# Kernel optimization log

Hardware: AMD Instinct MI355X
Metric: run time of the kernel (lower is better)

## Reference

```python
import jax, jax.numpy as jnp
import numpy as np

B, T, D, H = 8, 1024, 768, 12
HD = D // H          # 64 head dim
WINDOW = 768         # sliding-window width hardcoded in the block
EPS = 1e-5

def _layer_norm(x, w, b):
    mu = jnp.mean(x, axis=-1, keepdims=True)
    var = jnp.mean(jnp.square(x - mu), axis=-1, keepdims=True)
    return (x - mu) * jax.lax.rsqrt(var + EPS) * w + b

def setup_inputs() -> dict:
    key = jax.random.key(0)
    ks = jax.random.split(key, 16)
    s = 0.02
    return {
        "x": jax.random.normal(ks[0], (B, T, D), jnp.float32),
        "attn_mask": jnp.ones((B, T), jnp.int32),
        "ln1_w": jnp.ones((D,), jnp.float32),
        "ln1_b": jnp.zeros((D,), jnp.float32),
        "w_attn": jax.random.normal(ks[1], (D, 3 * D), jnp.float32) * s,
        "b_attn": jnp.zeros((3 * D,), jnp.float32),
        "w_proj": jax.random.normal(ks[2], (D, D), jnp.float32) * s,
        "b_proj": jnp.zeros((D,), jnp.float32),
        "ln2_w": jnp.ones((D,), jnp.float32),
        "ln2_b": jnp.zeros((D,), jnp.float32),
        "w_fc": jax.random.normal(ks[3], (D, 4 * D), jnp.float32) * s,
        "b_fc": jnp.zeros((4 * D,), jnp.float32),
        "w_fc_proj": jax.random.normal(ks[4], (4 * D, D), jnp.float32) * s,
        "b_fc_proj": jnp.zeros((D,), jnp.float32),
    }

def reference(x, attn_mask, ln1_w, ln1_b, w_attn, b_attn, w_proj, b_proj,
              ln2_w, ln2_b, w_fc, b_fc, w_fc_proj, b_fc_proj):
    dtype = x.dtype
    # --- attention sub-block ---
    x1 = _layer_norm(x, ln1_w, ln1_b)
    qkv = x1 @ w_attn + b_attn                       # [B,T,3D]
    q, k, v = jnp.split(qkv, 3, axis=-1)
    q = q.reshape(B, T, H, HD).transpose(0, 2, 1, 3)  # [B,H,T,HD]
    k = k.reshape(B, T, H, HD).transpose(0, 2, 1, 3)
    v = v.reshape(B, T, H, HD).transpose(0, 2, 1, 3)
    # causal + sliding-window + padding mask (additive bias, as in source)
    i = jnp.arange(T)[:, None]
    j = jnp.arange(T)[None, :]
    keep = (j <= i) & (j >= i - WINDOW + 1)           # [T,T]
    keep = keep[None, None] & (attn_mask.astype(bool))[:, None, None, :]  # [B,1,T,T]
    mask_bias = jnp.where(keep, jnp.zeros((), dtype), jnp.full((), jnp.finfo(dtype).min, dtype))
    scale = 1.0 / np.sqrt(HD)
    scores = jnp.einsum('bhqd,bhkd->bhqk', q, k) * scale + mask_bias
    probs = jax.nn.softmax(scores, axis=-1)
    attn = jnp.einsum('bhqk,bhkd->bhqd', probs, v)    # [B,H,T,HD]
    attn = attn.transpose(0, 2, 1, 3).reshape(B, T, D)
    a = attn @ w_proj + b_proj
    x = x + a
    # --- MLP sub-block ---
    x3 = _layer_norm(x, ln2_w, ln2_b)
    h = jax.nn.gelu(x3 @ w_fc + b_fc, approximate=False)
    m = h @ w_fc_proj + b_fc_proj
    return x + m
```

## Files before the change

kernel.cpp:

```cpp
#include <hip/hip_runtime.h>
#include <hip/hip_bf16.h>
#include <math.h>

#define NB 8
#define NT 1024
#define ND 768
#define NH 12
#define HD 64
#define WINDOW 768
#define LN_EPS 1e-5f
#define NEGF -3.4028234663852886e38f
#define SCL2 0.18033688011112042f

static const int BT = NB * NT;

typedef __bf16 bf16x8 __attribute__((ext_vector_type(8)));
typedef float  f32x4  __attribute__((ext_vector_type(4)));
typedef unsigned short ushort_t;

__device__ __forceinline__ unsigned short f2bf(float f) {
    __hip_bfloat16 h = __float2bfloat16(f);
    return __builtin_bit_cast(unsigned short, h);
}

__device__ __forceinline__ void load_lds16(const void* g, void* l) {
    __builtin_amdgcn_global_load_lds((const __attribute__((address_space(1))) unsigned int*)g,
                                     (__attribute__((address_space(3))) unsigned int*)l,
                                     16, 0, 0);
}

template <int IMM>
__device__ __forceinline__ bf16x8 ds_read16o(unsigned base) {
    bf16x8 r;
    asm volatile("ds_read_b128 %0, %1 offset:%2" : "=v"(r) : "v"(base), "n"(IMM));
    return r;
}

__global__ __launch_bounds__(256) void transpose_all(const float* __restrict__ w0, ushort_t* __restrict__ t0v,
                                                     const float* __restrict__ w1, ushort_t* __restrict__ t1v,
                                                     const float* __restrict__ w2, ushort_t* __restrict__ t2v,
                                                     const float* __restrict__ w3, ushort_t* __restrict__ t3v) {
    int bid = blockIdx.x;
    const float* w; ushort_t* wt; int K, N;
    if (bid < 1728)                    { w = w0; wt = t0v; K = 768;  N = 2304; }
    else if ((bid -= 1728) < 576)      { w = w1; wt = t1v; K = 768;  N = 768;  }
    else if ((bid -= 576) < 2304)      { w = w2; wt = t2v; K = 768;  N = 3072; }
    else       { bid -= 2304;            w = w3; wt = t3v; K = 3072; N = 768;  }
    const int nxt = N / 32;
    const int n0 = (bid % nxt) * 32, k0 = (bid / nxt) * 32;
    __shared__ float t[32][33];
    const int tx = threadIdx.x & 31, ty = threadIdx.x >> 5;
    for (int r = ty; r < 32; r += 8)
        t[r][tx] = w[(size_t)(k0 + r) * N + n0 + tx];
    __syncthreads();
    for (int r = ty; r < 32; r += 8)
        wt[(size_t)(n0 + r) * K + k0 + tx] = f2bf(t[tx][r]);
}

__global__ __launch_bounds__(256) void transpose_v(const ushort_t* __restrict__ qkvb,
                                                   ushort_t* __restrict__ vT) {
    const int t0 = blockIdx.x * 64;
    const int h = blockIdx.y, b = blockIdx.z;
    __shared__ ushort_t sm[64 * 72];
    const int tid = threadIdx.x;
    #pragma unroll
    for (int p = 0; p < 2; p++) {
        int idx = p * 256 + tid;
        int r = idx >> 3, c = idx & 7;
        *(bf16x8*)&sm[r * 72 + c * 8] =
            *(const bf16x8*)(qkvb + (size_t)(b * NT + t0 + r) * (3 * ND) + 2 * ND + h * HD + c * 8);
    }
    __syncthreads();
    #pragma unroll
    for (int p = 0; p < 2; p++) {
        int idx = p * 256 + tid;
        int d = idx >> 3, c2 = idx & 7;
        ushort_t tmp[8];
        #pragma unroll
        for (int j = 0; j < 8; j++) {
            int kp = c2 * 8 + j;
            int key = ((kp & 1) << 4) | ((kp >> 1) & 15) | (kp & 32);
            tmp[j] = sm[key * 72 + d];
        }
        *(bf16x8*)(vT + ((size_t)((b * NH + h) * HD + d)) * NT + t0 + c2 * 8) = *(bf16x8*)tmp;
    }
}

__global__ __launch_bounds__(256) void ln_kernel(const float* __restrict__ x,
                                                 const float* __restrict__ w,
                                                 const float* __restrict__ b,
                                                 ushort_t* __restrict__ out) {
    const int row  = blockIdx.x * 4 + (threadIdx.x >> 6);
    const int lane = threadIdx.x & 63;
    const float* xr = x + (size_t)row * ND;

    float4 v[3];
    #pragma unroll
    for (int s = 0; s < 3; s++) v[s] = *(const float4*)(xr + s * 256 + lane * 4);

    float sum = 0.f;
    #pragma unroll
    for (int s = 0; s < 3; s++) sum += v[s].x + v[s].y + v[s].z + v[s].w;
    #pragma unroll
    for (int off = 1; off < 64; off <<= 1) sum += __shfl_xor(sum, off, 64);
    const float mu = sum * (1.0f / ND);

    float var = 0.f;
    #pragma unroll
    for (int s = 0; s < 3; s++) {
        float a0 = v[s].x - mu, a1 = v[s].y - mu, a2 = v[s].z - mu, a3 = v[s].w - mu;
        var += a0 * a0 + a1 * a1 + a2 * a2 + a3 * a3;
    }
    #pragma unroll
    for (int off = 1; off < 64; off <<= 1) var += __shfl_xor(var, off, 64);
    const float rstd = rsqrtf(var * (1.0f / ND) + LN_EPS);

    #pragma unroll
    for (int s = 0; s < 3; s++) {
        const int col = s * 256 + lane * 4;
        float4 w4 = *(const float4*)(w + col);
        float4 b4 = *(const float4*)(b + col);
        ushort4 r;
        r.x = f2bf((v[s].x - mu) * rstd * w4.x + b4.x);
        r.y = f2bf((v[s].y - mu) * rstd * w4.y + b4.y);
        r.z = f2bf((v[s].z - mu) * rstd * w4.z + b4.z);
        r.w = f2bf((v[s].w - mu) * rstd * w4.w + b4.w);
        *(ushort4*)(out + (size_t)row * ND + col) = r;
    }
}

template <int EPI>
__global__ __launch_bounds__(256) void gemm_bt(const ushort_t* __restrict__ A,
                                               const ushort_t* __restrict__ Bt,
                                               const float* __restrict__ bias,
                                               const float* __restrict__ resid,
                                               void* __restrict__ Cout,
                                               int M, int N, int K) {
    __shared__ __align__(16) ushort_t smem[2][2][128 * 32];

    const int tid  = threadIdx.x;
    const int nwg   = gridDim.x * gridDim.y;
    const int flatb = blockIdx.y * gridDim.x + blockIdx.x;
    const int q8    = nwg >> 3;
    const int swz   = (flatb & 7) * q8 + (flatb >> 3);
    const int bm   = (swz / gridDim.x) * 128;
    const int bn   = (swz % gridDim.x) * 128;
    const int lane = tid & 63;
    const int wave = tid >> 6;
    const int wm   = (wave & 1) * 64;
    const int wn   = (wave >> 1) * 64;
    const int fcol = lane & 15;
    const int quad = lane >> 4;

    f32x4 acc[4][4] = {};

    const int srow = tid >> 2, scg = (tid & 3) * 8;

    auto issue = [&](int k0, int buf) {
        #pragma unroll
        for (int p = 0; p < 2; p++) {
            const int row = srow + p * 64;
            const int flat = (p * 256 + tid) * 8;
            load_lds16(A  + (size_t)(bm + row) * K + k0 + scg, &smem[buf][0][flat]);
            load_lds16(Bt + (size_t)(bn + row) * K + k0 + scg, &smem[buf][1][flat]);
        }
    };

    issue(0, 0);
    const int KT = K >> 5;
    for (int kt = 0; kt < KT; kt++) {
        const int cur = kt & 1;
        __syncthreads();
        if (kt + 1 < KT) issue((kt + 1) << 5, cur ^ 1);

        bf16x8 a[4], b[4];
        #pragma unroll
        for (int i = 0; i < 4; i++)
            a[i] = *(const bf16x8*)&smem[cur][0][(wm + i * 16 + fcol) * 32 + quad * 8];
        #pragma unroll
        for (int j = 0; j < 4; j++)
            b[j] = *(const bf16x8*)&smem[cur][1][(wn + j * 16 + fcol) * 32 + quad * 8];
        #pragma unroll
        for (int i = 0; i < 4; i++)
            #pragma unroll
            for (int j = 0; j < 4; j++)
                acc[i][j] = __builtin_amdgcn_mfma_f32_16x16x32_bf16(a[i], b[j], acc[i][j], 0, 0, 0);
    }

    if (EPI == 1) {
        #pragma unroll
        for (int j = 0; j < 4; j++) {
            const int gcol = bn + wn + j * 16 + fcol;
            const float bs = bias[gcol];
            #pragma unroll
            for (int i = 0; i < 4; i++) {
                #pragma unroll
                for (int r = 0; r < 4; r++) {
                    const int grow = bm + wm + i * 16 + quad * 4 + r;
                    float val = acc[i][j][r] + bs + resid[(size_t)grow * N + gcol];
                    ((float*)Cout)[(size_t)grow * N + gcol] = val;
                }
            }
        }
    } else {
        __syncthreads();
        ushort_t* Cs = &smem[0][0][0] + wave * (64 * 40);
        #pragma unroll
        for (int hh = 0; hh < 2; hh++) {
            #pragma unroll
            for (int jj = 0; jj < 2; jj++) {
                const int j = hh * 2 + jj;
                const float bs = bias[bn + wn + j * 16 + fcol];
                #pragma unroll
                for (int i = 0; i < 4; i++) {
                    #pragma unroll
                    for (int r = 0; r < 4; r++) {
                        float val = acc[i][j][r] + bs;
                        if (EPI == 2) {
                            float y = 0.7978845608028654f * (val + 0.044715f * val * val * val);
                            float t = 1.0f - 2.0f / (1.0f + __expf(2.0f * y));
                            val = 0.5f * val * (1.0f + t);
                        }
                        const int lr = i * 16 + quad * 4 + r;
                        Cs[lr * 40 + jj * 16 + fcol] = f2bf(val);
                    }
                }
            }
            #pragma unroll
            for (int p = 0; p < 4; p++) {
                const int cid = p * 64 + lane;
                const int lr = cid >> 2, ck = cid & 3;
                bf16x8 vv = *(const bf16x8*)&Cs[lr * 40 + ck * 8];
                *(bf16x8*)((ushort_t*)Cout + (size_t)(bm + wm + lr) * N + bn + wn + hh * 32 + ck * 8) = vv;
            }
        }
    }
}

template <int EPI, int NN, int KK>
__global__ __launch_bounds__(512, 4) void gemm128n(const ushort_t* __restrict__ A,
                                                   const ushort_t* __restrict__ Bt,
                                                   const float* __restrict__ bias,
                                                   ushort_t* __restrict__ Cout) {
    __shared__ __align__(16) ushort_t lds[24576];

    const int tid  = threadIdx.x;
    const int lane = tid & 63;
    const int wave = tid >> 6;
    const int wr   = wave >> 2;
    const int wn   = wave & 3;
    const int fcol = lane & 15;
    const int quad = lane >> 4;

    const int nwg   = gridDim.x * gridDim.y;
    const int flatb = blockIdx.y * gridDim.x + blockIdx.x;
    const int q8    = nwg >> 3;
    const int swz   = (flatb & 7) * q8 + (flatb >> 3);
    const int bm    = (swz / gridDim.x) * 128;
    const int bn    = (swz % gridDim.x) * 256;

    constexpr int KTILES = KK >> 5;

    f32x4 acc[4][4] = {};
    bf16x8 ra[4], rbv[4];

    const unsigned ldsb = (unsigned)(size_t)(const __attribute__((address_space(3))) ushort_t*)lds;
    const unsigned slotr = (unsigned)(((((fcol & 1) << 2) | quad) ^ (fcol >> 1)) * 16);
    const unsigned baseA = ldsb + (unsigned)((wr * 32 + (fcol >> 1)) * 128) + slotr;
    const unsigned baseB = ldsb + 16384u + (unsigned)((wn * 32 + (fcol >> 1)) * 128) + slotr;

    auto stage = [&](int kt) {
        const int kk = (kt < KTILES ? kt : 0) << 5;
        ushort_t* dstA = lds + (kt & 1) * 4096;
        {
            const int f = tid;
            const int pr = f >> 3, s2 = (f & 7) ^ (pr & 7);
            const int r = pr * 2 + (s2 >> 2), c = s2 & 3;
            load_lds16(A + (size_t)(bm + r) * KK + kk + c * 8, dstA + f * 8);
        }
        ushort_t* dstB = lds + 8192 + (kt & 1) * 8192;
        #pragma unroll
        for (int p = 0; p < 2; p++) {
            const int f = (p << 9) + tid;
            const int pr = f >> 3, s2 = (f & 7) ^ (pr & 7);
            const int r = pr * 2 + (s2 >> 2), c = s2 & 3;
            load_lds16(Bt + (size_t)(bn + r) * KK + kk + c * 8, dstB + f * 8);
        }
    };

#define RD_T(CUR) {                                                        \
    ra[0]  = ds_read16o<(CUR) * 8192 + 0   >(baseA);                       \
    ra[1]  = ds_read16o<(CUR) * 8192 + 1024>(baseA);                       \
    ra[2]  = ds_read16o<(CUR) * 8192 + 2048>(baseA);                       \
    ra[3]  = ds_read16o<(CUR) * 8192 + 3072>(baseA);                       \
    rbv[0] = ds_read16o<(CUR) * 16384 + 0   >(baseB);                      \
    rbv[1] = ds_read16o<(CUR) * 16384 + 1024>(baseB);                      \
    rbv[2] = ds_read16o<(CUR) * 16384 + 2048>(baseB);                      \
    rbv[3] = ds_read16o<(CUR) * 16384 + 3072>(baseB); }
#define LGKM0() { asm volatile("s_waitcnt lgkmcnt(0)" ::: "memory");       \
    __builtin_amdgcn_sched_barrier(0); }
#define MMA16() {                                                          \
    __builtin_amdgcn_s_setprio(1);                                         \
    _Pragma("unroll") for (int i = 0; i < 4; i++)                          \
    _Pragma("unroll") for (int j = 0; j < 4; j++)                          \
        acc[i][j] = __builtin_amdgcn_mfma_f32_16x16x32_bf16(               \
            ra[i], rbv[j], acc[i][j], 0, 0, 0);                            \
    __builtin_amdgcn_s_setprio(0);                                         \
    __builtin_amdgcn_sched_barrier(0); }
#define VMW3() asm volatile("s_waitcnt vmcnt(3)" ::: "memory")
#define BARR() asm volatile("s_barrier" ::: "memory")

    stage(0); stage(1);
    VMW3();
    BARR();

    #pragma unroll 1
    for (int it = 0; it < KTILES / 2; ++it) {
        const int t = it << 1;
        RD_T(0);
        LGKM0();
        MMA16();
        BARR();
        stage(t + 2);
        VMW3();
        BARR();
        RD_T(1);
        LGKM0();
        MMA16();
        BARR();
        stage(t + 3);
        VMW3();
        BARR();
    }

    asm volatile("s_waitcnt vmcnt(0) lgkmcnt(0)" ::: "memory");
    BARR();

    ushort_t* Cs = lds + wave * (32 * 72);
    #pragma unroll
    for (int h = 0; h < 2; h++) {
        #pragma unroll
        for (int j = 0; j < 4; j++) {
            const float bs = bias[bn + wn * 64 + j * 16 + fcol];
            #pragma unroll
            for (int i2 = 0; i2 < 2; i2++) {
                #pragma unroll
                for (int r = 0; r < 4; r++) {
                    float val = acc[h * 2 + i2][j][r] + bs;
                    if (EPI == 2) {
                        float y = 0.7978845608028654f * (val + 0.044715f * val * val * val);
                        float t = 1.0f - 2.0f / (1.0f + __expf(2.0f * y));
                        val = 0.5f * val * (1.0f + t);
                    }
                    Cs[(i2 * 16 + quad * 4 + r) * 72 + j * 16 + fcol] = f2bf(val);
                }
            }
        }
        __builtin_amdgcn_sched_barrier(0);
        #pragma unroll
        for (int p = 0; p < 4; p++) {
            const int cid = (p << 6) + lane;
            const int lr = cid >> 3, ck = cid & 7;
            bf16x8 vv = *(const bf16x8*)&Cs[lr * 72 + ck * 8];
            *(bf16x8*)(Cout + (size_t)(bm + wr * 64 + h * 32 + lr) * NN + bn + wn * 64 + ck * 8) = vv;
        }
        __builtin_amdgcn_sched_barrier(0);
    }
#undef RD_T
#undef LGKM0
#undef MMA16
#undef VMW3
#undef BARR
}

__global__ __launch_bounds__(256) void flash_attn_mfma(const ushort_t* __restrict__ qkvb,
                                                       const ushort_t* __restrict__ vT,
                                                       const int* __restrict__ amask,
                                                       ushort_t* __restrict__ out) {
    const int qt = 15 - blockIdx.x;
    const int h  = blockIdx.y;
    const int b  = blockIdx.z;
    const int q0 = qt * 64;

    __shared__ __align__(16) ushort_t QPs[64 * 64];
    __shared__ __align__(16) ushort_t Ks[2][64 * 64];
    __shared__ __align__(16) ushort_t Vts[2][64 * 64];

    const int tid  = threadIdx.x;
    const int lane = tid & 63;
    const int wave = tid >> 6;
    const int fcol = lane & 15;
    const int quad = lane >> 4;
    const int wq0  = wave * 16;

    #pragma unroll
    for (int p = 0; p < 2; p++) {
        int flat = p * 256 + tid;
        int r = flat >> 3, c = (flat & 7) ^ (r & 7);
        load_lds16(qkvb + (size_t)(b * NT + q0 + r) * (3 * ND) + h * HD + c * 8, &QPs[flat * 8]);
    }
    __syncthreads();

    bf16x8 aQ[2];
    {
        const int qr = wq0 + fcol;
        #pragma unroll
        for (int ks = 0; ks < 2; ks++) {
            int c = ks * 4 + quad;
            aQ[ks] = *(const bf16x8*)&QPs[qr * 64 + ((c ^ (qr & 7)) * 8)];
        }
    }

    bf16x8 bones;
    #pragma unroll
    for (int i = 0; i < 8; i++) bones[i] = (__bf16)1.0f;

    auto issueKV = [&](int cch, int buf) {
        const int kbase = cch * 64;
        #pragma unroll
        for (int p = 0; p < 2; p++) {
            int flat = p * 256 + tid;
            int r = flat >> 3, c = (flat & 7) ^ (r & 7);
            load_lds16(qkvb + (size_t)(b * NT + kbase + r) * (3 * ND) + ND + h * HD + c * 8,
                       &Ks[buf][flat * 8]);
            load_lds16(vT + ((size_t)((b * NH + h) * HD + r)) * NT + kbase + c * 8,
                       &Vts[buf][flat * 8]);
        }
    };

    f32x4 oacc[4] = {};
    f32x4 lacc = {};

    const int c_lo = (qt > 12) ? (qt - 12) : 0;
    issueKV(c_lo, 0);
    for (int cch = c_lo; cch <= qt; cch++) {
        const int cur = (cch - c_lo) & 1;
        const int kbase = cch * 64;
        __syncthreads();
        if (cch + 1 <= qt) issueKV(cch + 1, cur ^ 1);

        int am[4];
        #pragma unroll
        for (int jn = 0; jn < 4; jn++) am[jn] = amask[b * NT + kbase + jn * 16 + fcol];
        const int amok_lane = (am[0] != 0) & (am[1] != 0) & (am[2] != 0) & (am[3] != 0);
        const bool fast = (cch < qt) && (cch >= qt - 11) && __all(amok_lane);

        f32x4 sc[4] = {};
        #pragma unroll
        for (int ks = 0; ks < 2; ks++) {
            #pragma unroll
            for (int jn = 0; jn < 4; jn++) {
                const int kr = jn * 16 + fcol;
                bf16x8 bk = *(const bf16x8*)&Ks[cur][kr * 64 + (((ks * 4 + quad) ^ (kr & 7)) * 8)];
                sc[jn] = __builtin_amdgcn_mfma_f32_16x16x32_bf16(aQ[ks], bk, sc[jn], 0, 0, 0);
            }
        }

        float pvv[4][4];
        if (fast) {
            #pragma unroll
            for (int jn = 0; jn < 4; jn++)
                #pragma unroll
                for (int r = 0; r < 4; r++)
                    pvv[jn][r] = __builtin_amdgcn_exp2f(sc[jn][r] * SCL2);
        } else {
            #pragma unroll
            for (int jn = 0; jn < 4; jn++) {
                const int jg = kbase + jn * 16 + fcol;
                const bool amok = (am[jn] != 0);
                #pragma unroll
                for (int r = 0; r < 4; r++) {
                    const int ig = q0 + wq0 + quad * 4 + r;
                    bool keep = (jg <= ig) && (jg >= ig - (WINDOW - 1)) && amok;
                    float s = keep ? sc[jn][r] * SCL2 : -1e38f;
                    pvv[jn][r] = __builtin_amdgcn_exp2f(s);
                }
            }
        }

        #pragma unroll
        for (int half = 0; half < 2; half++) {
            const int cbase = half * 4 + (fcol >> 2);
            const int off = (fcol & 3) * 2;
            #pragma unroll
            for (int r = 0; r < 4; r++) {
                const int row = wq0 + quad * 4 + r;
                unsigned int pk = (unsigned int)f2bf(pvv[half * 2][r]) |
                                  ((unsigned int)f2bf(pvv[half * 2 + 1][r]) << 16);
                *(unsigned int*)&QPs[row * 64 + ((cbase ^ (row & 7)) * 8) + off] = pk;
            }
        }

        #pragma unroll
        for (int ks = 0; ks < 2; ks++) {
            const int pr = wq0 + fcol;
            bf16x8 ap = *(const bf16x8*)&QPs[pr * 64 + (((ks * 4 + quad) ^ (pr & 7)) * 8)];
            lacc = __builtin_amdgcn_mfma_f32_16x16x32_bf16(ap, bones, lacc, 0, 0, 0);
            #pragma unroll
            for (int jd = 0; jd < 4; jd++) {
                const int vr = jd * 16 + fcol;
                bf16x8 bv = *(const bf16x8*)&Vts[cur][vr * 64 + (((ks * 4 + quad) ^ (vr & 7)) * 8)];
                oacc[jd] = __builtin_amdgcn_mfma_f32_16x16x32_bf16(ap, bv, oacc[jd], 0, 0, 0);
            }
        }
    }

    #pragma unroll
    for (int r = 0; r < 4; r++) {
        const float inv = 1.0f / lacc[r];
        const size_t row = (size_t)(b * NT + q0 + wq0 + quad * 4 + r);
        #pragma unroll
        for (int jd = 0; jd < 4; jd++)
            out[row * ND + h * HD + jd * 16 + fcol] = f2bf(oacc[jd][r] * inv);
    }
}

extern "C" void kernel_launch(void* const* d_in, const int* in_sizes, int n_in,
                              void* d_out, int out_size, void* d_ws, size_t ws_size,
                              hipStream_t stream) {
    const float* x        = (const float*)d_in[0];
    const int*   amask    = (const int*)  d_in[1];
    const float* ln1_w    = (const float*)d_in[2];
    const float* ln1_b    = (const float*)d_in[3];
    const float* w_attn   = (const float*)d_in[4];
    const float* b_attn   = (const float*)d_in[5];
    const float* w_proj   = (const float*)d_in[6];
    const float* b_proj   = (const float*)d_in[7];
    const float* ln2_w    = (const float*)d_in[8];
    const float* ln2_b    = (const float*)d_in[9];
    const float* w_fc     = (const float*)d_in[10];
    const float* b_fc     = (const float*)d_in[11];
    const float* w_fcp    = (const float*)d_in[12];
    const float* b_fcp    = (const float*)d_in[13];
    float* out = (float*)d_out;

    ushort_t* ws = (ushort_t*)d_ws;
    ushort_t* qkvb   = ws;
    ushort_t* x1b    = qkvb + (size_t)BT * 3 * ND;
    ushort_t* attn_b = x1b + (size_t)BT * ND;
    ushort_t* hbuf   = attn_b + (size_t)BT * ND;
    ushort_t* vTb    = hbuf + (size_t)BT * 4 * ND;
    ushort_t* wA_T   = vTb + (size_t)BT * ND;
    ushort_t* wP_T   = wA_T + (size_t)2304 * 768;
    ushort_t* wF_T   = wP_T + (size_t)768 * 768;
    ushort_t* wFP_T  = wF_T + (size_t)3072 * 768;

    transpose_all<<<6912, 256, 0, stream>>>(w_attn, wA_T, w_proj, wP_T, w_fc, wF_T, w_fcp, wFP_T);

    ln_kernel<<<BT / 4, 256, 0, stream>>>(x, ln1_w, ln1_b, x1b);
    gemm128n<0, 2304, 768><<<dim3(2304 / 256, BT / 128), 512, 0, stream>>>(x1b, wA_T, b_attn, qkvb);
    transpose_v<<<dim3(16, NH, NB), 256, 0, stream>>>(qkvb, vTb);
    flash_attn_mfma<<<dim3(16, NH, NB), 256, 0, stream>>>(qkvb, vTb, amask, attn_b);
    gemm_bt<1><<<dim3(768 / 128, BT / 128), 256, 0, stream>>>(attn_b, wP_T, b_proj, x, out, BT, ND, ND);
    ln_kernel<<<BT / 4, 256, 0, stream>>>(out, ln2_w, ln2_b, x1b);
    gemm128n<2, 3072, 768><<<dim3(3072 / 256, BT / 128), 512, 0, stream>>>(x1b, wF_T, b_fc, hbuf);
    gemm_bt<1><<<dim3(768 / 128, BT / 128), 256, 0, stream>>>(hbuf, wFP_T, b_fcp, out, out, BT, ND, 4 * ND);
}
```

Measured before the change: 358.5 us.

## Triple-buffer gemm128n LDS pipeline and XOR-swizzle LDS layout in gemm128

In gemm128n the double-buffered K-loop becomes a three-stage ring, with LDS grown to hold three A/B tiles and the vmcnt wait relaxed from 3 to 6. This keeps two tiles of global loads in flight while the MFMAs run. Separately, the 128x128 gemm kernel adopts the same XOR-swizzled pair-row LDS layout for staging and fragment reads, to cut LDS bank conflicts. The extra LDS in gemm128n may lower occupancy. The loop now assumes KTILES is divisible by 3, which holds for K=768 (24 tiles) and K=3072 (96 tiles).

```diff
diff --git a/kernel.cpp b/kernel.cpp
--- a/kernel.cpp
+++ b/kernel.cpp
@@ -154,17 +154,18 @@
 
     f32x4 acc[4][4] = {};
 
-    const int srow = tid >> 2, scg = (tid & 3) * 8;
-
     auto issue = [&](int k0, int buf) {
         #pragma unroll
         for (int p = 0; p < 2; p++) {
-            const int row = srow + p * 64;
-            const int flat = (p * 256 + tid) * 8;
-            load_lds16(A  + (size_t)(bm + row) * K + k0 + scg, &smem[buf][0][flat]);
-            load_lds16(Bt + (size_t)(bn + row) * K + k0 + scg, &smem[buf][1][flat]);
+            const int f = p * 256 + tid;
+            const int pr = f >> 3, s2 = (f & 7) ^ (pr & 7);
+            const int r = pr * 2 + (s2 >> 2), c = s2 & 3;
+            load_lds16(A  + (size_t)(bm + r) * K + k0 + c * 8, &smem[buf][0][f * 8]);
+            load_lds16(Bt + (size_t)(bn + r) * K + k0 + c * 8, &smem[buf][1][f * 8]);
         }
     };
+
+    const int slr = ((((fcol & 1) << 2) | quad) ^ (fcol >> 1)) * 8;
 
     issue(0, 0);
     const int KT = K >> 5;
@@ -176,10 +177,10 @@
         bf16x8 a[4], b[4];
         #pragma unroll
         for (int i = 0; i < 4; i++)
-            a[i] = *(const bf16x8*)&smem[cur][0][(wm + i * 16 + fcol) * 32 + quad * 8];
+            a[i] = *(const bf16x8*)&smem[cur][0][((wm + i * 16 + fcol) >> 1) * 64 + slr];
         #pragma unroll
         for (int j = 0; j < 4; j++)
-            b[j] = *(const bf16x8*)&smem[cur][1][(wn + j * 16 + fcol) * 32 + quad * 8];
+            b[j] = *(const bf16x8*)&smem[cur][1][((wn + j * 16 + fcol) >> 1) * 64 + slr];
         #pragma unroll
         for (int i = 0; i < 4; i++)
             #pragma unroll
@@ -242,7 +243,7 @@
                                                    const ushort_t* __restrict__ Bt,
                                                    const float* __restrict__ bias,
                                                    ushort_t* __restrict__ Cout) {
-    __shared__ __align__(16) ushort_t lds[24576];
+    __shared__ __align__(16) ushort_t lds[36864];
 
     const int tid  = threadIdx.x;
     const int lane = tid & 63;
@@ -267,18 +268,18 @@
     const unsigned ldsb = (unsigned)(size_t)(const __attribute__((address_space(3))) ushort_t*)lds;
     const unsigned slotr = (unsigned)(((((fcol & 1) << 2) | quad) ^ (fcol >> 1)) * 16);
     const unsigned baseA = ldsb + (unsigned)((wr * 32 + (fcol >> 1)) * 128) + slotr;
-    const unsigned baseB = ldsb + 16384u + (unsigned)((wn * 32 + (fcol >> 1)) * 128) + slotr;
-
-    auto stage = [&](int kt) {
+    const unsigned baseB = ldsb + 24576u + (unsigned)((wn * 32 + (fcol >> 1)) * 128) + slotr;
+
+    auto stage = [&](int kt, int slot) {
         const int kk = (kt < KTILES ? kt : 0) << 5;
-        ushort_t* dstA = lds + (kt & 1) * 4096;
+        ushort_t* dstA = lds + slot * 4096;
         {
             const int f = tid;
             const int pr = f >> 3, s2 = (f & 7) ^ (pr & 7);
             const int r = pr * 2 + (s2 >> 2), c = s2 & 3;
             load_lds16(A + (size_t)(bm + r) * KK + kk + c * 8, dstA + f * 8);
         }
-        ushort_t* dstB = lds + 8192 + (kt & 1) * 8192;
+        ushort_t* dstB = lds + 12288 + slot * 8192;
         #pragma unroll
         for (int p = 0; p < 2; p++) {
             const int f = (p << 9) + tid;
@@ -307,29 +308,36 @@
             ra[i], rbv[j], acc[i][j], 0, 0, 0);                            \
     __builtin_amdgcn_s_setprio(0);                                         \
     __builtin_amdgcn_sched_barrier(0); }
-#define VMW3() asm volatile("s_waitcnt vmcnt(3)" ::: "memory")
+#define VMW6() asm volatile("s_waitcnt vmcnt(6)" ::: "memory")
 #define BARR() asm volatile("s_barrier" ::: "memory")
 
-    stage(0); stage(1);
-    VMW3();
+    stage(0, 0); stage(1, 1); stage(2, 2);
+    VMW6();
     BARR();
 
     #pragma unroll 1
-    for (int it = 0; it < KTILES / 2; ++it) {
-        const int t = it << 1;
+    for (int it = 0; it < KTILES / 3; ++it) {
+        const int t = it * 3;
         RD_T(0);
         LGKM0();
         MMA16();
         BARR();
-        stage(t + 2);
-        VMW3();
+        stage(t + 3, 0);
+        VMW6();
         BARR();
         RD_T(1);
         LGKM0();
         MMA16();
         BARR();
-        stage(t + 3);
-        VMW3();
+        stage(t + 4, 1);
+        VMW6();
+        BARR();
+        RD_T(2);
+        LGKM0();
+        MMA16();
+        BARR();
+        stage(t + 5, 2);
+        VMW6();
         BARR();
     }
 
@@ -369,7 +377,7 @@
 #undef RD_T
 #undef LGKM0
 #undef MMA16
-#undef VMW3
+#undef VMW6
 #undef BARR
 }
 
```

Measured after the change: 350.4 us. 2.2% less time.
